# Kernel optimization log

Hardware: AMD Instinct MI355X
Metric: run time of the kernel (lower is better)

## Reference

```python
import jax, jax.numpy as jnp
import numpy as np

B, N, D = 32, 4096, 512
HID = 64
MIN_K, MAX_K = 3, 50
IN_DIM = 3 * D + 5  # mean/max/std pooled features + 5 structural features
NEG_SENTINEL = -1e8


def setup_inputs() -> dict:
    key = jax.random.key(0)
    ks = jax.random.split(key, 9)
    x = jax.random.normal(ks[0], (B, N, D), dtype=jnp.float32)
    keep = jax.random.uniform(ks[1], (B, 1, N)) < 0.75
    mask = jnp.where(keep, 0.0, -1e9).astype(jnp.float32)
    def lin(k, fan_in, fan_out):
        bound = 1.0 / np.sqrt(fan_in)
        kw, kb = jax.random.split(k)
        W = jax.random.uniform(kw, (fan_in, fan_out), minval=-bound, maxval=bound, dtype=jnp.float32)
        b = jax.random.uniform(kb, (fan_out,), minval=-bound, maxval=bound, dtype=jnp.float32)
        return W, b
    W1, b1 = lin(ks[2], IN_DIM, HID)
    W2, b2 = lin(ks[3], HID, HID // 2)
    W3, b3 = lin(ks[4], HID // 2, 1)
    return {"x": x, "mask": mask, "W1": W1, "b1": b1, "W2": W2, "b2": b2, "W3": W3, "b3": b3}


def reference(x, mask, W1, b1, W2, b2, W3, b3):
    valid = mask[:, 0, :] > NEG_SENTINEL            # [B, N] bool
    m = valid.astype(x.dtype)[..., None]            # [B, N, 1]
    cnt = m.sum(axis=1)                             # [B, 1] valid-node counts
    cnt_safe = jnp.maximum(cnt, 1.0)
    has_nodes = cnt > 0.0                           # [B, 1]

    # masked mean / max / unbiased std pooling (segment-reduce over nodes)
    x_mean = (x * m).sum(axis=1) / cnt_safe                                    # [B, D]
    x_mean = jnp.where(has_nodes, x_mean, 0.0)
    x_max = jnp.where(valid[..., None], x, -jnp.inf).max(axis=1)               # [B, D]
    x_max = jnp.where(has_nodes, x_max, 0.0)
    var = (m * (x - x_mean[:, None, :]) ** 2).sum(axis=1) / jnp.maximum(cnt - 1.0, 1.0)
    x_std = jnp.where(has_nodes, jnp.sqrt(var), 0.0)                           # [B, D]

    # structural features: dense path with no edge_index -> constants except log_size
    n = cnt[:, 0]
    log_size = jnp.log(n + 1.0) / 5.0
    ones = jnp.ones_like(log_size)
    # [log_size, density=0.1, avg_degree/10=0.2, max_degree=4.0, degree_std/10=0.1]
    sf = jnp.stack([log_size, 0.1 * ones, 0.2 * ones, 4.0 * ones, 0.1 * ones], axis=1)  # [B, 5]

    g = jnp.concatenate([x_mean, x_max, x_std, sf], axis=1)   # [B, 3D+5]
    h = jax.nn.relu(g @ W1 + b1)                              # dropout is identity in eval
    h = jax.nn.relu(h @ W2 + b2)
    score = jax.nn.sigmoid(h @ W3 + b3)[:, 0]                 # [B]

    num_clusters_cont = MIN_K + score * (MAX_K - MIN_K)
    num_clusters = jnp.round(num_clusters_cont).mean().astype(jnp.int32)
    num_clusters = jnp.clip(num_clusters, MIN_K, MAX_K)
    return num_clusters, score.mean()
```

## Files before the change

### kernel.cpp

```cpp
#include <hip/hip_runtime.h>
#include <cmath>

#define B_      32
#define N_      4096
#define D_      512
#define D4      (D_/4)
#define NCH     32
#define RPC     128
#define IN_DIM  1541
#define GSTRIDE 1568
#define NSPLIT  8
#define CHUNK   193
#define NEG_SENT (-1.0e8f)
#define BIGNEG   (1.0e30f)

__global__ __launch_bounds__(128) void stats_partial_kernel(
    const float* __restrict__ x, const float* __restrict__ mask,
    float4* __restrict__ psum, float4* __restrict__ psq,
    float4* __restrict__ pmax, float* __restrict__ pcnt)
{
    __shared__ int sidx[RPC];
    __shared__ int swc0, swc1;
    const int tx   = threadIdx.x;
    const int wave = tx >> 6;
    const int lane = tx & 63;
    const int c    = blockIdx.x;
    const int b    = blockIdx.y;

    {
        const float mv = mask[b * N_ + c * RPC + tx];
        const bool pred = mv > NEG_SENT;
        const unsigned long long bal = __ballot(pred);
        const int prefix = __popcll(bal & ((1ull << lane) - 1ull));
        if (lane == 0) { if (wave == 0) swc0 = __popcll(bal); else swc1 = __popcll(bal); }
        __syncthreads();
        const int base = (wave == 0) ? 0 : swc0;
        if (pred) sidx[base + prefix] = tx;
    }
    __syncthreads();
    const int m = swc0 + swc1;
    if (tx == 0) pcnt[b * NCH + c] = (float)m;

    const float4* __restrict__ xb =
        (const float4*)x + ((size_t)b * N_ + (size_t)c * RPC) * D4 + tx;

    float4 s  = {0,0,0,0};
    float4 q  = {0,0,0,0};
    float4 mx = {-BIGNEG,-BIGNEG,-BIGNEG,-BIGNEG};

    #pragma unroll 4
    for (int i = 0; i < m; ++i) {
        const int r = sidx[i];
        const float4 v = xb[(size_t)r * D4];
        s.x += v.x; s.y += v.y; s.z += v.z; s.w += v.w;
        q.x = fmaf(v.x, v.x, q.x); q.y = fmaf(v.y, v.y, q.y);
        q.z = fmaf(v.z, v.z, q.z); q.w = fmaf(v.w, v.w, q.w);
        mx.x = fmaxf(mx.x, v.x); mx.y = fmaxf(mx.y, v.y);
        mx.z = fmaxf(mx.z, v.z); mx.w = fmaxf(mx.w, v.w);
    }

    const size_t idx = ((size_t)(b * NCH + c)) * D4 + tx;
    psum[idx] = s; psq[idx] = q; pmax[idx] = mx;
}

__global__ __launch_bounds__(256) void combine_g_kernel(
    const float4* __restrict__ psum, const float4* __restrict__ psq,
    const float4* __restrict__ pmax, const float* __restrict__ pcnt,
    float* __restrict__ g_all)
{
    __shared__ float4 Ss[2][D4], Sq[2][D4], Sm[2][D4];
    __shared__ float scnt;

    const int tid = threadIdx.x;
    const int tx  = tid & 127;
    const int ty  = tid >> 7;
    const int b   = blockIdx.x;

    {
        float4 s = {0,0,0,0}, q = {0,0,0,0};
        float4 mx = {-BIGNEG,-BIGNEG,-BIGNEG,-BIGNEG};
        const int c0 = ty * (NCH/2);
        #pragma unroll 4
        for (int c = c0; c < c0 + NCH/2; ++c) {
            const size_t idx = ((size_t)(b * NCH + c)) * D4 + tx;
            float4 a = psum[idx], u = psq[idx], w = pmax[idx];
            s.x += a.x; s.y += a.y; s.z += a.z; s.w += a.w;
            q.x += u.x; q.y += u.y; q.z += u.z; q.w += u.w;
            mx.x = fmaxf(mx.x,w.x); mx.y = fmaxf(mx.y,w.y);
            mx.z = fmaxf(mx.z,w.z); mx.w = fmaxf(mx.w,w.w);
        }
        Ss[ty][tx] = s; Sq[ty][tx] = q; Sm[ty][tx] = mx;
    }
    if (tid < NCH) {
        float cv = pcnt[b * NCH + tid];
        #pragma unroll
        for (int off = 16; off > 0; off >>= 1) cv += __shfl_down(cv, off);
        if (tid == 0) scnt = cv;
    }
    __syncthreads();

    const float cnt = scnt;
    float* __restrict__ g = g_all + (size_t)b * GSTRIDE;
    if (ty == 0) {
        float4 s = Ss[0][tx], s_ = Ss[1][tx];
        float4 q = Sq[0][tx], q_ = Sq[1][tx];
        float4 mx = Sm[0][tx], m_ = Sm[1][tx];
        s.x += s_.x; s.y += s_.y; s.z += s_.z; s.w += s_.w;
        q.x += q_.x; q.y += q_.y; q.z += q_.z; q.w += q_.w;
        mx.x = fmaxf(mx.x,m_.x); mx.y = fmaxf(mx.y,m_.y);
        mx.z = fmaxf(mx.z,m_.z); mx.w = fmaxf(mx.w,m_.w);

        const bool  has = cnt > 0.f;
        const float inv = 1.f / fmaxf(cnt, 1.f);
        const float dn  = 1.f / fmaxf(cnt - 1.f, 1.f);
        float sa[4] = {s.x,s.y,s.z,s.w};
        float qa[4] = {q.x,q.y,q.z,q.w};
        float ma[4] = {mx.x,mx.y,mx.z,mx.w};
        #pragma unroll
        for (int k = 0; k < 4; ++k) {
            const int d = 4*tx + k;
            const float mn = has ? sa[k] * inv : 0.f;
            const float vv = fmaxf((qa[k] - cnt * mn * mn) * dn, 0.f);
            g[d]        = mn;
            g[D_ + d]   = has ? ma[k] : 0.f;
            g[2*D_ + d] = has ? sqrtf(vv) : 0.f;
        }
        if (tx == 0) {
            g[3*D_ + 0] = logf(cnt + 1.f) * 0.2f;
            g[3*D_ + 1] = 0.1f;
            g[3*D_ + 2] = 0.2f;
            g[3*D_ + 3] = 4.0f;
            g[3*D_ + 4] = 0.1f;
        }
    }
}

__global__ __launch_bounds__(64) void layer1_kernel(
    const float* __restrict__ g_all, const float* __restrict__ W1,
    float* __restrict__ h1p)
{
    __shared__ float sg[CHUNK];
    const int o  = threadIdx.x;
    const int c  = blockIdx.x;
    const int b  = blockIdx.y;
    const int i0 = c * CHUNK;
    const int len = (IN_DIM - i0) < CHUNK ? (IN_DIM - i0) : CHUNK;

    for (int j = o; j < len; j += 64) sg[j] = g_all[(size_t)b * GSTRIDE + i0 + j];
    __syncthreads();

    const float* __restrict__ Wp = W1 + (size_t)i0 * 64 + o;
    float a = 0.f;
    #pragma unroll 8
    for (int k = 0; k < len; ++k)
        a = fmaf(sg[k], Wp[(size_t)k * 64], a);
    h1p[((size_t)b * NSPLIT + c) * 64 + o] = a;
}

__global__ __launch_bounds__(1024) void finish_kernel(
    const float* __restrict__ h1p, const float* __restrict__ b1,
    const float* __restrict__ W2, const float* __restrict__ b2,
    const float* __restrict__ W3, const float* __restrict__ b3,
    float* __restrict__ out)
{
    __shared__ float h1s[B_ * 64];
    __shared__ float h2s[B_ * 33];
    const int tid = threadIdx.x;

    #pragma unroll
    for (int r = 0; r < 2; ++r) {
        const int oi = tid + r * 1024;
        const int b = oi >> 6, o = oi & 63;
        float a = b1[o];
        #pragma unroll
        for (int c = 0; c < NSPLIT; ++c) a += h1p[((size_t)b * NSPLIT + c) * 64 + o];
        h1s[oi] = fmaxf(a, 0.f);
    }
    __syncthreads();

    {
        const int b = tid >> 5, o = tid & 31;
        float a = b2[o];
        #pragma unroll
        for (int i = 0; i < 64; ++i) a = fmaf(h1s[b*64 + i], W2[i*32 + o], a);
        h2s[b*33 + o] = fmaxf(a, 0.f);
    }
    __syncthreads();

    if (tid < 32) {
        const int b = tid;
        float a = b3[0];
        #pragma unroll
        for (int i = 0; i < 32; ++i) a = fmaf(h2s[b*33 + i], W3[i], a);
        float sc = 1.f / (1.f + expf(-a));
        float r  = rintf(3.f + sc * 47.f);
        #pragma unroll
        for (int off = 16; off > 0; off >>= 1) {
            sc += __shfl_down(sc, off);
            r  += __shfl_down(r,  off);
        }
        if (tid == 0) {
            const float mean_r = r * (1.f / 32.f);
            int nc = (int)mean_r;
            nc = nc < 3 ? 3 : (nc > 50 ? 50 : nc);
            out[0] = (float)nc;
            out[1] = sc * (1.f / 32.f);
        }
    }
}

extern "C" void kernel_launch(void* const* d_in, const int* in_sizes, int n_in,
                              void* d_out, int out_size, void* d_ws, size_t ws_size,
                              hipStream_t stream)
{
    const float* x    = (const float*)d_in[0];
    const float* mask = (const float*)d_in[1];
    const float* W1   = (const float*)d_in[2];
    const float* b1   = (const float*)d_in[3];
    const float* W2   = (const float*)d_in[4];
    const float* b2   = (const float*)d_in[5];
    const float* W3   = (const float*)d_in[6];
    const float* b3   = (const float*)d_in[7];
    float* out = (float*)d_out;

    const size_t PCOUNT = (size_t)B_ * NCH * D4;
    float4* psum = (float4*)d_ws;
    float4* psq  = psum + PCOUNT;
    float4* pmax = psq  + PCOUNT;
    float*  pcnt = (float*)(pmax + PCOUNT);
    float*  g_all = pcnt + (size_t)B_ * NCH;
    float*  h1p   = g_all + (size_t)B_ * GSTRIDE;

    dim3 gridA(NCH, B_);
    stats_partial_kernel<<<gridA, 128, 0, stream>>>(x, mask, psum, psq, pmax, pcnt);
    combine_g_kernel<<<B_, 256, 0, stream>>>(psum, psq, pmax, pcnt, g_all);
    dim3 gridL1(NSPLIT, B_);
    layer1_kernel<<<gridL1, 64, 0, stream>>>(g_all, W1, h1p);
    finish_kernel<<<1, 1024, 0, stream>>>(h1p, b1, W2, b2, W3, b3, out);
}
```

Baseline: 380.3 us.

## Fuse layer1 into combine kernel and widen stats blocks to float2 lanes

The stats kernel now runs 256 threads per block, with each thread reading float2 instead of float4, to raise the number of in-flight loads per block. The combine step keeps the pooled feature vector in shared memory and computes the first-layer partial dot products itself, which removes one kernel launch and the global round-trip of g. The compaction step now contains a redundant first ballot pass with a stray write into sidx, and the fused layer1 runs only 32 blocks, so it has less parallelism than the separate kernel had.

```diff
diff --git a/kernel.cpp b/kernel.cpp
--- a/kernel.cpp
+++ b/kernel.cpp
@@ -5,71 +5,79 @@
 #define N_      4096
 #define D_      512
 #define D4      (D_/4)
+#define D2      (D_/2)
 #define NCH     32
 #define RPC     128
 #define IN_DIM  1541
-#define GSTRIDE 1568
 #define NSPLIT  8
 #define CHUNK   193
 #define NEG_SENT (-1.0e8f)
 #define BIGNEG   (1.0e30f)
 
-__global__ __launch_bounds__(128) void stats_partial_kernel(
+__global__ __launch_bounds__(256) void stats_partial_kernel(
     const float* __restrict__ x, const float* __restrict__ mask,
-    float4* __restrict__ psum, float4* __restrict__ psq,
-    float4* __restrict__ pmax, float* __restrict__ pcnt)
+    float2* __restrict__ psum, float2* __restrict__ psq,
+    float2* __restrict__ pmax, float* __restrict__ pcnt)
 {
     __shared__ int sidx[RPC];
     __shared__ int swc0, swc1;
-    const int tx   = threadIdx.x;
-    const int wave = tx >> 6;
-    const int lane = tx & 63;
+    const int tid  = threadIdx.x;
     const int c    = blockIdx.x;
     const int b    = blockIdx.y;
 
-    {
-        const float mv = mask[b * N_ + c * RPC + tx];
+    if (tid < RPC) {
+        const int wave = tid >> 6;
+        const int lane = tid & 63;
+        const float mv = mask[b * N_ + c * RPC + tid];
         const bool pred = mv > NEG_SENT;
         const unsigned long long bal = __ballot(pred);
         const int prefix = __popcll(bal & ((1ull << lane) - 1ull));
         if (lane == 0) { if (wave == 0) swc0 = __popcll(bal); else swc1 = __popcll(bal); }
-        __syncthreads();
+        if (pred) sidx[(wave == 0 ? 0 : __popcll(__ballot(pred)) ) ] = 0;
+    }
+    __syncthreads();
+    if (tid < RPC) {
+        const int wave = tid >> 6;
+        const int lane = tid & 63;
+        const float mv = mask[b * N_ + c * RPC + tid];
+        const bool pred = mv > NEG_SENT;
+        const unsigned long long bal = __ballot(pred);
+        const int prefix = __popcll(bal & ((1ull << lane) - 1ull));
         const int base = (wave == 0) ? 0 : swc0;
-        if (pred) sidx[base + prefix] = tx;
+        if (pred) sidx[base + prefix] = tid;
     }
     __syncthreads();
     const int m = swc0 + swc1;
-    if (tx == 0) pcnt[b * NCH + c] = (float)m;
-
-    const float4* __restrict__ xb =
-        (const float4*)x + ((size_t)b * N_ + (size_t)c * RPC) * D4 + tx;
-
-    float4 s  = {0,0,0,0};
-    float4 q  = {0,0,0,0};
-    float4 mx = {-BIGNEG,-BIGNEG,-BIGNEG,-BIGNEG};
-
-    #pragma unroll 4
+    if (tid == 0) pcnt[b * NCH + c] = (float)m;
+
+    const float2* __restrict__ xb =
+        (const float2*)x + ((size_t)b * N_ + (size_t)c * RPC) * D2 + tid;
+
+    float2 s  = {0.f, 0.f};
+    float2 q  = {0.f, 0.f};
+    float2 mx = {-BIGNEG, -BIGNEG};
+
+    #pragma unroll 8
     for (int i = 0; i < m; ++i) {
         const int r = sidx[i];
-        const float4 v = xb[(size_t)r * D4];
-        s.x += v.x; s.y += v.y; s.z += v.z; s.w += v.w;
+        const float2 v = xb[(size_t)r * D2];
+        s.x += v.x; s.y += v.y;
         q.x = fmaf(v.x, v.x, q.x); q.y = fmaf(v.y, v.y, q.y);
-        q.z = fmaf(v.z, v.z, q.z); q.w = fmaf(v.w, v.w, q.w);
-        mx.x = fmaxf(mx.x, v.x); mx.y = fmaxf(mx.y, v.y);
-        mx.z = fmaxf(mx.z, v.z); mx.w = fmaxf(mx.w, v.w);
-    }
-
-    const size_t idx = ((size_t)(b * NCH + c)) * D4 + tx;
+        mx.x = fmaxf(mx.x, v.x);   mx.y = fmaxf(mx.y, v.y);
+    }
+
+    const size_t idx = ((size_t)(b * NCH + c)) * D2 + tid;
     psum[idx] = s; psq[idx] = q; pmax[idx] = mx;
 }
 
-__global__ __launch_bounds__(256) void combine_g_kernel(
+__global__ __launch_bounds__(256) void combine_layer1_kernel(
     const float4* __restrict__ psum, const float4* __restrict__ psq,
     const float4* __restrict__ pmax, const float* __restrict__ pcnt,
-    float* __restrict__ g_all)
+    const float* __restrict__ W1, float* __restrict__ h1p)
 {
     __shared__ float4 Ss[2][D4], Sq[2][D4], Sm[2][D4];
     __shared__ float scnt;
+    __shared__ float gsh[IN_DIM];
 
     const int tid = threadIdx.x;
     const int tx  = tid & 127;
@@ -100,7 +108,6 @@
     __syncthreads();
 
     const float cnt = scnt;
-    float* __restrict__ g = g_all + (size_t)b * GSTRIDE;
     if (ty == 0) {
         float4 s = Ss[0][tx], s_ = Ss[1][tx];
         float4 q = Sq[0][tx], q_ = Sq[1][tx];
@@ -121,40 +128,36 @@
             const int d = 4*tx + k;
             const float mn = has ? sa[k] * inv : 0.f;
             const float vv = fmaxf((qa[k] - cnt * mn * mn) * dn, 0.f);
-            g[d]        = mn;
-            g[D_ + d]   = has ? ma[k] : 0.f;
-            g[2*D_ + d] = has ? sqrtf(vv) : 0.f;
+            gsh[d]        = mn;
+            gsh[D_ + d]   = has ? ma[k] : 0.f;
+            gsh[2*D_ + d] = has ? sqrtf(vv) : 0.f;
         }
         if (tx == 0) {
-            g[3*D_ + 0] = logf(cnt + 1.f) * 0.2f;
-            g[3*D_ + 1] = 0.1f;
-            g[3*D_ + 2] = 0.2f;
-            g[3*D_ + 3] = 4.0f;
-            g[3*D_ + 4] = 0.1f;
-        }
-    }
-}
-
-__global__ __launch_bounds__(64) void layer1_kernel(
-    const float* __restrict__ g_all, const float* __restrict__ W1,
-    float* __restrict__ h1p)
-{
-    __shared__ float sg[CHUNK];
-    const int o  = threadIdx.x;
-    const int c  = blockIdx.x;
-    const int b  = blockIdx.y;
-    const int i0 = c * CHUNK;
-    const int len = (IN_DIM - i0) < CHUNK ? (IN_DIM - i0) : CHUNK;
-
-    for (int j = o; j < len; j += 64) sg[j] = g_all[(size_t)b * GSTRIDE + i0 + j];
-    __syncthreads();
-
-    const float* __restrict__ Wp = W1 + (size_t)i0 * 64 + o;
-    float a = 0.f;
-    #pragma unroll 8
-    for (int k = 0; k < len; ++k)
-        a = fmaf(sg[k], Wp[(size_t)k * 64], a);
-    h1p[((size_t)b * NSPLIT + c) * 64 + o] = a;
+            gsh[3*D_ + 0] = logf(cnt + 1.f) * 0.2f;
+            gsh[3*D_ + 1] = 0.1f;
+            gsh[3*D_ + 2] = 0.2f;
+            gsh[3*D_ + 3] = 4.0f;
+            gsh[3*D_ + 4] = 0.1f;
+        }
+    }
+    __syncthreads();
+
+    {
+        const int o = tid & 63;
+        const int p = tid >> 6;
+        #pragma unroll
+        for (int cc = 0; cc < 2; ++cc) {
+            const int c  = p + cc * 4;
+            const int i0 = c * CHUNK;
+            const int len = (IN_DIM - i0) < CHUNK ? (IN_DIM - i0) : CHUNK;
+            const float* __restrict__ Wp = W1 + (size_t)i0 * 64 + o;
+            float a = 0.f;
+            #pragma unroll 8
+            for (int k = 0; k < len; ++k)
+                a = fmaf(gsh[i0 + k], Wp[(size_t)k * 64], a);
+            h1p[((size_t)b * NSPLIT + c) * 64 + o] = a;
+        }
+    }
 }
 
 __global__ __launch_bounds__(1024) void finish_kernel(
@@ -223,18 +226,16 @@
     const float* b3   = (const float*)d_in[7];
     float* out = (float*)d_out;
 
-    const size_t PCOUNT = (size_t)B_ * NCH * D4;
-    float4* psum = (float4*)d_ws;
-    float4* psq  = psum + PCOUNT;
-    float4* pmax = psq  + PCOUNT;
-    float*  pcnt = (float*)(pmax + PCOUNT);
-    float*  g_all = pcnt + (size_t)B_ * NCH;
-    float*  h1p   = g_all + (size_t)B_ * GSTRIDE;
+    const size_t PCOUNT2 = (size_t)B_ * NCH * D2;
+    float2* psum = (float2*)d_ws;
+    float2* psq  = psum + PCOUNT2;
+    float2* pmax = psq  + PCOUNT2;
+    float*  pcnt = (float*)(pmax + PCOUNT2);
+    float*  h1p  = pcnt + (size_t)B_ * NCH;
 
     dim3 gridA(NCH, B_);
-    stats_partial_kernel<<<gridA, 128, 0, stream>>>(x, mask, psum, psq, pmax, pcnt);
-    combine_g_kernel<<<B_, 256, 0, stream>>>(psum, psq, pmax, pcnt, g_all);
-    dim3 gridL1(NSPLIT, B_);
-    layer1_kernel<<<gridL1, 64, 0, stream>>>(g_all, W1, h1p);
+    stats_partial_kernel<<<gridA, 256, 0, stream>>>(x, mask, psum, psq, pmax, pcnt);
+    combine_layer1_kernel<<<B_, 256, 0, stream>>>(
+        (const float4*)psum, (const float4*)psq, (const float4*)pmax, pcnt, W1, h1p);
     finish_kernel<<<1, 1024, 0, stream>>>(h1p, b1, W2, b2, W3, b3, out);
 }
```

Result: no change. 387.2 us (+1.8%).
